# Kernel tuning notes

Hardware: AMD Instinct MI355X
Metric: run time of the kernel (lower is better)

## Reference

```python
import jax, jax.numpy as jnp
import numpy as np

B, TDIM, NDIM, KDIM, VDIM, FDIM, ODIM = 128, 256, 128, 128, 128, 2048, 32


def setup_inputs() -> dict:
    key = jax.random.key(0)
    ks = jax.random.split(key, 14)
    s = 0.02  # small init so sigmoids are not saturated
    return {
        "X":  jax.random.normal(ks[0], (B, TDIM, NDIM), dtype=jnp.float32),
        "Qw": jax.random.normal(ks[1], (NDIM, KDIM), dtype=jnp.float32) * s,
        "Qb": jnp.zeros((KDIM,), dtype=jnp.float32),
        "Kw": jax.random.normal(ks[2], (NDIM, KDIM), dtype=jnp.float32) * s,
        "Kb": jnp.zeros((KDIM,), dtype=jnp.float32),
        "Vw": jax.random.normal(ks[3], (NDIM, VDIM), dtype=jnp.float32) * s,
        "Vb": jnp.zeros((VDIM,), dtype=jnp.float32),
        "W1": jax.random.normal(ks[4], (TDIM * VDIM, FDIM), dtype=jnp.float32) * s,
        "b1": jnp.zeros((FDIM,), dtype=jnp.float32),
        "W2": jax.random.normal(ks[5], (FDIM, FDIM), dtype=jnp.float32) * s,
        "b2": jnp.zeros((FDIM,), dtype=jnp.float32),
        "W3": jax.random.normal(ks[6], (FDIM, ODIM * NDIM), dtype=jnp.float32) * s,
        "b3": jnp.zeros((ODIM * NDIM,), dtype=jnp.float32),
    }


def reference(X, Qw, Qb, Kw, Kb, Vw, Vb, W1, b1, W2, b2, W3, b3):
    # projections [B, T, kdim/vdim]
    q = X @ Qw + Qb
    k = X @ Kw + Kb
    v = X @ Vw + Vb
    # NOTE: original computes softmax(K Q^T) with NO 1/sqrt(d) scaling
    scores = jnp.einsum("btk,bsk->bts", k, q)        # [B, T, T]
    a = jax.nn.softmax(scores, axis=-1)
    r = jnp.einsum("bts,bsv->btv", a, v)              # [B, T, V]
    r = r.reshape(-1, TDIM * VDIM)                    # [B, T*V]
    h = jax.nn.sigmoid(r @ W1 + b1)
    h = jax.nn.sigmoid(h @ W2 + b2)
    return h @ W3 + b3                                # [B, ODIM*NDIM]
```

## Files before the change

kernel.cpp:

```cpp
#include <hip/hip_runtime.h>


#define DI __device__ __forceinline__
#define AS1 __attribute__((address_space(1)))
#define AS3 __attribute__((address_space(3)))

typedef __attribute__((ext_vector_type(4))) float f32x4;
typedef __attribute__((ext_vector_type(8))) short bf16x8;

DI unsigned short f2bf(float f) {
  unsigned int u = __float_as_uint(f);
  u += 0x7fffu + ((u >> 16) & 1u);
  return (unsigned short)(u >> 16);
}

__global__ __launch_bounds__(256) void prep_wt(const float* __restrict__ Qw,
                                               const float* __restrict__ Kw,
                                               const float* __restrict__ Vw,
                                               unsigned short* __restrict__ wT) {
  int gid = blockIdx.x * 256 + threadIdx.x;
  int w  = gid >> 14;
  int j  = gid & 16383;
  int no = j >> 7, ni = j & 127;
  const float* src = (w == 0) ? Qw : (w == 1) ? Kw : Vw;
  wT[gid] = f2bf(src[ni * 128 + no]);
}

__global__ __launch_bounds__(256) void proj_kernel(
    const float* __restrict__ X, const unsigned short* __restrict__ wT,
    const float* __restrict__ Qb, const float* __restrict__ Kb,
    const float* __restrict__ Vb,
    unsigned short* __restrict__ q_ws, unsigned short* __restrict__ k_ws,
    unsigned short* __restrict__ vT_ws) {
  int wv = threadIdx.x >> 6, lane = threadIdx.x & 63;
  int quad = lane >> 4, l15 = lane & 15;
  int R0 = blockIdx.x * 64 + wv * 16;

  bf16x8 af[4];
  const float* xbase = X + (size_t)(R0 + l15) * 128 + quad * 8;
#pragma unroll
  for (int kc = 0; kc < 4; ++kc) {
    f32x4 x0 = *(const f32x4*)(xbase + kc * 32);
    f32x4 x1 = *(const f32x4*)(xbase + kc * 32 + 4);
    bf16x8 a;
#pragma unroll
    for (int j = 0; j < 4; ++j) { a[j] = (short)f2bf(x0[j]); a[4 + j] = (short)f2bf(x1[j]); }
    af[kc] = a;
  }

#pragma unroll
  for (int p = 0; p < 3; ++p) {
    const unsigned short* wt = wT + p * 16384;
    const float* bias = (p == 0) ? Qb : (p == 1) ? Kb : Vb;
#pragma unroll
    for (int nt = 0; nt < 8; ++nt) {
      f32x4 acc = {0.f, 0.f, 0.f, 0.f};
#pragma unroll
      for (int kc = 0; kc < 4; ++kc) {
        bf16x8 b = *(const bf16x8*)(wt + (size_t)(nt * 16 + l15) * 128 + kc * 32 + quad * 8);
        acc = __builtin_amdgcn_mfma_f32_16x16x32_bf16(af[kc], b, acc, 0, 0, 0);
      }
      int no = nt * 16 + l15;
      float bv = bias[no];
#pragma unroll
      for (int r4 = 0; r4 < 4; ++r4) {
        int row = R0 + quad * 4 + r4;
        unsigned short val = f2bf(acc[r4] + bv);
        if (p == 0)      q_ws[(size_t)row * 128 + no] = val;
        else if (p == 1) k_ws[(size_t)row * 128 + no] = val;
        else {
          int bb = row >> 8, t = row & 255;
          vT_ws[((size_t)bb * 128 + no) * 256 + t] = val;
        }
      }
    }
  }
}

__global__ __launch_bounds__(256) void attn_kernel(
    const unsigned short* __restrict__ q_ws, const unsigned short* __restrict__ k_ws,
    const unsigned short* __restrict__ vT_ws, unsigned short* __restrict__ r_ws) {
  __shared__ __align__(16) unsigned short p_lds[4][16 * 264];
  int wv = threadIdx.x >> 6, lane = threadIdx.x & 63;
  int quad = lane >> 4, l15 = lane & 15;
  int b  = blockIdx.x >> 2;
  int t0 = (blockIdx.x & 3) * 64 + wv * 16;

  bf16x8 kf[4];
  const unsigned short* kbase = k_ws + ((size_t)b * 256 + t0 + l15) * 128 + quad * 8;
#pragma unroll
  for (int kc = 0; kc < 4; ++kc) kf[kc] = *(const bf16x8*)(kbase + kc * 32);

  f32x4 sc[16];
#pragma unroll
  for (int st = 0; st < 16; ++st) {
    f32x4 acc = {0.f, 0.f, 0.f, 0.f};
    const unsigned short* qbase = q_ws + ((size_t)b * 256 + st * 16 + l15) * 128 + quad * 8;
#pragma unroll
    for (int kc = 0; kc < 4; ++kc) {
      bf16x8 qf = *(const bf16x8*)(qbase + kc * 32);
      acc = __builtin_amdgcn_mfma_f32_16x16x32_bf16(kf[kc], qf, acc, 0, 0, 0);
    }
    sc[st] = acc;
  }

  float inv[4];
#pragma unroll
  for (int r4 = 0; r4 < 4; ++r4) {
    float m = sc[0][r4];
#pragma unroll
    for (int st = 1; st < 16; ++st) m = fmaxf(m, sc[st][r4]);
#pragma unroll
    for (int d = 1; d < 16; d <<= 1) m = fmaxf(m, __shfl_xor(m, d, 64));
    float s = 0.f;
#pragma unroll
    for (int st = 0; st < 16; ++st) { float e = __expf(sc[st][r4] - m); sc[st][r4] = e; s += e; }
#pragma unroll
    for (int d = 1; d < 16; d <<= 1) s += __shfl_xor(s, d, 64);
    inv[r4] = 1.f / s;
  }

#pragma unroll
  for (int st = 0; st < 16; ++st)
#pragma unroll
    for (int r4 = 0; r4 < 4; ++r4)
      p_lds[wv][(quad * 4 + r4) * 264 + st * 16 + l15] = f2bf(sc[st][r4] * inv[r4]);
  __syncthreads();

  const unsigned short* pbase = &p_lds[wv][l15 * 264 + quad * 8];
#pragma unroll
  for (int vt = 0; vt < 8; ++vt) {
    f32x4 acc = {0.f, 0.f, 0.f, 0.f};
    const unsigned short* vbase = vT_ws + ((size_t)b * 128 + vt * 16 + l15) * 256 + quad * 8;
#pragma unroll
    for (int s8 = 0; s8 < 8; ++s8) {
      bf16x8 pf = *(const bf16x8*)(pbase + s8 * 32);
      bf16x8 vf = *(const bf16x8*)(vbase + s8 * 32);
      acc = __builtin_amdgcn_mfma_f32_16x16x32_bf16(pf, vf, acc, 0, 0, 0);
    }
#pragma unroll
    for (int r4 = 0; r4 < 4; ++r4)
      r_ws[((size_t)b * 256 + t0 + quad * 4 + r4) * 128 + vt * 16 + l15] = f2bf(acc[r4]);
  }
}

__global__ __launch_bounds__(256) void gemm_ksplit(
    const unsigned short* __restrict__ A, int lda,
    const float* __restrict__ B, int ldb,
    float* __restrict__ slab, int ldo, int nChunks) {
  __shared__ __align__(16) unsigned short bt[2][128 * 32];
  const int tid  = threadIdx.x;
  const int wv   = tid >> 6, lane = tid & 63;
  const int quad = lane >> 4, l15 = lane & 15;
  const int n0   = blockIdx.x * 128;
  const long k0  = (long)blockIdx.y * nChunks * 32;
  const int m0   = wv * 32;

  const int kp = tid >> 4;
  const int nq = tid & 15;
  const int gq = kp >> 2;
  const int qd = kp & 3;

  f32x4 acc[2][8];
#pragma unroll
  for (int ms = 0; ms < 2; ++ms)
#pragma unroll
    for (int nt = 0; nt < 8; ++nt) acc[ms][nt] = (f32x4){0.f, 0.f, 0.f, 0.f};

  f32x4 r0, r1, r2, r3;
  auto LOAD = [&](int c) {
    const float* g = B + (size_t)(k0 + c * 32 + 2 * kp) * (size_t)ldb + n0 + nq * 8;
    r0 = *(const f32x4*)(g);
    r1 = *(const f32x4*)(g + 4);
    r2 = *(const f32x4*)(g + ldb);
    r3 = *(const f32x4*)(g + ldb + 4);
  };
  auto WRITE = [&](int pb) {
#pragma unroll
    for (int i = 0; i < 8; ++i) {
      int n = nq * 8 + i;
      float lo = (i < 4) ? r0[i] : r1[i - 4];
      float hi = (i < 4) ? r2[i] : r3[i - 4];
      unsigned int pk = (unsigned int)f2bf(lo) | ((unsigned int)f2bf(hi) << 16);
      int d = ((n >> 1) & 3) ^ ((n >> 3) & 3);
      *(unsigned int*)&bt[pb][n * 32 + ((gq ^ d) << 3) + 2 * qd] = pk;
    }
  };

  const int rb = l15 * 64 + ((quad ^ ((l15 >> 1) & 3) ^ (l15 >> 3)) << 4);

  LOAD(0);
  WRITE(0);
  __syncthreads();

  for (int c = 0; c < nChunks; ++c) {
    const int pb = c & 1;
    if (c + 1 < nChunks) LOAD(c + 1);

    bf16x8 aF[2];
    const unsigned short* abase = A + (size_t)(m0 + l15) * lda + k0 + c * 32 + quad * 8;
    aF[0] = *(const bf16x8*)(abase);
    aF[1] = *(const bf16x8*)(abase + (size_t)16 * lda);

    const char* be = (const char*)&bt[pb][0] + rb;
    const char* bo = (const char*)&bt[pb][0] + (rb ^ 32);
#pragma unroll
    for (int nt = 0; nt < 8; ++nt) {
      bf16x8 bF = *(const bf16x8*)(((nt & 1) ? bo : be) + nt * 1024);
      acc[0][nt] = __builtin_amdgcn_mfma_f32_16x16x32_bf16(aF[0], bF, acc[0][nt], 0, 0, 0);
      acc[1][nt] = __builtin_amdgcn_mfma_f32_16x16x32_bf16(aF[1], bF, acc[1][nt], 0, 0, 0);
    }
    __syncthreads();
    if (c + 1 < nChunks) {
      WRITE(pb ^ 1);
      __syncthreads();
    }
  }

  float* out = slab + (size_t)blockIdx.y * (size_t)ldo * 128;
#pragma unroll
  for (int ms = 0; ms < 2; ++ms)
#pragma unroll
    for (int nt = 0; nt < 8; ++nt)
#pragma unroll
      for (int r4 = 0; r4 < 4; ++r4)
        out[(size_t)(m0 + ms * 16 + quad * 4 + r4) * ldo + n0 + nt * 16 + l15] =
            acc[ms][nt][r4];
}

__global__ __launch_bounds__(256) void reduce_sig(
    const float* __restrict__ slabs, int nslabs, int slabStride,
    const float* __restrict__ bias, int biasMask, unsigned short* __restrict__ outBf) {
  int i = blockIdx.x * 256 + threadIdx.x;
  float s = 0.f;
  for (int y = 0; y < nslabs; ++y) s += slabs[(size_t)y * slabStride + i];
  s += bias[i & biasMask];
  outBf[i] = f2bf(1.f / (1.f + __expf(-s)));
}

__global__ __launch_bounds__(256) void reduce_bias_out(
    const float* __restrict__ slabs, int nslabs, int slabStride,
    const float* __restrict__ bias, int biasMask, float* __restrict__ outF) {
  int i = blockIdx.x * 256 + threadIdx.x;
  float s = 0.f;
  for (int y = 0; y < nslabs; ++y) s += slabs[(size_t)y * slabStride + i];
  outF[i] = s + bias[i & biasMask];
}

extern "C" void kernel_launch(void* const* d_in, const int* in_sizes, int n_in,
                              void* d_out, int out_size, void* d_ws, size_t ws_size,
                              hipStream_t stream) {
  const float* X  = (const float*)d_in[0];
  const float* Qw = (const float*)d_in[1];
  const float* Qb = (const float*)d_in[2];
  const float* Kw = (const float*)d_in[3];
  const float* Kb = (const float*)d_in[4];
  const float* Vw = (const float*)d_in[5];
  const float* Vb = (const float*)d_in[6];
  const float* W1 = (const float*)d_in[7];
  const float* b1 = (const float*)d_in[8];
  const float* W2 = (const float*)d_in[9];
  const float* b2 = (const float*)d_in[10];
  const float* W3 = (const float*)d_in[11];
  const float* b3 = (const float*)d_in[12];

  char* ws = (char*)d_ws;
  unsigned short* wT    = (unsigned short*)(ws + 0);
  unsigned short* r_ws  = (unsigned short*)(ws + 98304);
  unsigned short* q_ws  = (unsigned short*)(ws + 8486912);
  unsigned short* k_ws  = (unsigned short*)(ws + 16875520);
  unsigned short* vT_ws = (unsigned short*)(ws + 25264128);
  float* g1 = (float*)(ws + 8486912);
  unsigned short* h1bf = (unsigned short*)(ws + 42041344);
  float* g2 = (float*)(ws + 8486912);
  unsigned short* h2bf = (unsigned short*)(ws + 42565632);
  float* g3 = (float*)(ws + 8486912);

  prep_wt<<<192, 256, 0, stream>>>(Qw, Kw, Vw, wT);
  proj_kernel<<<512, 256, 0, stream>>>(X, wT, Qb, Kb, Vb, q_ws, k_ws, vT_ws);
  attn_kernel<<<512, 256, 0, stream>>>(q_ws, k_ws, vT_ws, r_ws);
  gemm_ksplit<<<dim3(16, 32), 256, 0, stream>>>(r_ws, 32768, W1, 2048, g1, 2048, 32);
  reduce_sig<<<1024, 256, 0, stream>>>(g1, 32, 262144, b1, 2047, h1bf);
  gemm_ksplit<<<dim3(16, 16), 256, 0, stream>>>(h1bf, 2048, W2, 2048, g2, 2048, 4);
  reduce_sig<<<1024, 256, 0, stream>>>(g2, 16, 262144, b2, 2047, h2bf);
  gemm_ksplit<<<dim3(32, 16), 256, 0, stream>>>(h2bf, 2048, W3, 4096, g3, 4096, 4);
  reduce_bias_out<<<2048, 256, 0, stream>>>(g3, 16, 524288, b3, 4095, (float*)d_out);
}
```

Before: 517.3 us.

## Software-pipeline ksplit GEMM two chunks deep and double W2 k-split

The ksplit GEMM main loop is unrolled by two. It keeps separate register sets for even and odd chunks and prefetches both the A fragments and the B tile two chunks ahead. Plain __syncthreads are replaced by lgkmcnt waits plus raw s_barrier with scheduling fences. The aim is to overlap global loads with MFMA work and to stop the A-fragment loads from stalling the math. The W2 GEMM also moves to 32 k-splits of 2 chunks each for more blocks, at the cost of a larger slab reduction. The loop assumes an even chunk count, and the weaker barriers rely on the manual waitcnt for correctness.

```diff
diff --git a/kernel.cpp b/kernel.cpp
--- a/kernel.cpp
+++ b/kernel.cpp
@@ -2,8 +2,6 @@
 
 
 #define DI __device__ __forceinline__
-#define AS1 __attribute__((address_space(1)))
-#define AS3 __attribute__((address_space(3)))
 
 typedef __attribute__((ext_vector_type(4))) float f32x4;
 typedef __attribute__((ext_vector_type(8))) short bf16x8;
@@ -161,61 +159,85 @@
   const int gq = kp >> 2;
   const int qd = kp & 3;
 
+  const int rb_ = l15 * 64 + ((quad ^ ((l15 >> 1) & 3) ^ (l15 >> 3)) << 4);
+
   f32x4 acc[2][8];
 #pragma unroll
   for (int ms = 0; ms < 2; ++ms)
 #pragma unroll
     for (int nt = 0; nt < 8; ++nt) acc[ms][nt] = (f32x4){0.f, 0.f, 0.f, 0.f};
 
-  f32x4 r0, r1, r2, r3;
-  auto LOAD = [&](int c) {
+  f32x4 e0, e1, e2, e3;
+  f32x4 o0, o1, o2, o3;
+  bf16x8 ae0, ae1;
+  bf16x8 ao0, ao1;
+
+  auto LOADB = [&](int c, f32x4& s0, f32x4& s1, f32x4& s2, f32x4& s3) {
     const float* g = B + (size_t)(k0 + c * 32 + 2 * kp) * (size_t)ldb + n0 + nq * 8;
-    r0 = *(const f32x4*)(g);
-    r1 = *(const f32x4*)(g + 4);
-    r2 = *(const f32x4*)(g + ldb);
-    r3 = *(const f32x4*)(g + ldb + 4);
+    s0 = *(const f32x4*)(g);
+    s1 = *(const f32x4*)(g + 4);
+    s2 = *(const f32x4*)(g + ldb);
+    s3 = *(const f32x4*)(g + ldb + 4);
   };
-  auto WRITE = [&](int pb) {
+  auto LOADA = [&](int c, bf16x8& a0, bf16x8& a1) {
+    const unsigned short* abase = A + (size_t)(m0 + l15) * lda + k0 + c * 32 + quad * 8;
+    a0 = *(const bf16x8*)(abase);
+    a1 = *(const bf16x8*)(abase + (size_t)16 * lda);
+  };
+  auto WRITE = [&](int pb, const f32x4& s0, const f32x4& s1, const f32x4& s2,
+                   const f32x4& s3) {
 #pragma unroll
     for (int i = 0; i < 8; ++i) {
       int n = nq * 8 + i;
-      float lo = (i < 4) ? r0[i] : r1[i - 4];
-      float hi = (i < 4) ? r2[i] : r3[i - 4];
+      float lo = (i < 4) ? s0[i] : s1[i - 4];
+      float hi = (i < 4) ? s2[i] : s3[i - 4];
       unsigned int pk = (unsigned int)f2bf(lo) | ((unsigned int)f2bf(hi) << 16);
       int d = ((n >> 1) & 3) ^ ((n >> 3) & 3);
       *(unsigned int*)&bt[pb][n * 32 + ((gq ^ d) << 3) + 2 * qd] = pk;
     }
   };
-
-  const int rb = l15 * 64 + ((quad ^ ((l15 >> 1) & 3) ^ (l15 >> 3)) << 4);
-
-  LOAD(0);
-  WRITE(0);
-  __syncthreads();
-
-  for (int c = 0; c < nChunks; ++c) {
-    const int pb = c & 1;
-    if (c + 1 < nChunks) LOAD(c + 1);
-
-    bf16x8 aF[2];
-    const unsigned short* abase = A + (size_t)(m0 + l15) * lda + k0 + c * 32 + quad * 8;
-    aF[0] = *(const bf16x8*)(abase);
-    aF[1] = *(const bf16x8*)(abase + (size_t)16 * lda);
-
-    const char* be = (const char*)&bt[pb][0] + rb;
-    const char* bo = (const char*)&bt[pb][0] + (rb ^ 32);
+  auto MFMA8 = [&](int pb, const bf16x8& a0, const bf16x8& a1) {
+    const char* be = (const char*)&bt[pb][0] + rb_;
+    const char* bo = (const char*)&bt[pb][0] + (rb_ ^ 32);
 #pragma unroll
     for (int nt = 0; nt < 8; ++nt) {
       bf16x8 bF = *(const bf16x8*)(((nt & 1) ? bo : be) + nt * 1024);
-      acc[0][nt] = __builtin_amdgcn_mfma_f32_16x16x32_bf16(aF[0], bF, acc[0][nt], 0, 0, 0);
-      acc[1][nt] = __builtin_amdgcn_mfma_f32_16x16x32_bf16(aF[1], bF, acc[1][nt], 0, 0, 0);
-    }
-    __syncthreads();
-    if (c + 1 < nChunks) {
-      WRITE(pb ^ 1);
-      __syncthreads();
-    }
-  }
+      acc[0][nt] = __builtin_amdgcn_mfma_f32_16x16x32_bf16(a0, bF, acc[0][nt], 0, 0, 0);
+      acc[1][nt] = __builtin_amdgcn_mfma_f32_16x16x32_bf16(a1, bF, acc[1][nt], 0, 0, 0);
+    }
+  };
+
+#define BAR_LGKM()                                   \
+  asm volatile("s_waitcnt lgkmcnt(0)" ::: "memory"); \
+  __builtin_amdgcn_sched_barrier(0);                 \
+  __builtin_amdgcn_s_barrier();                      \
+  __builtin_amdgcn_sched_barrier(0)
+
+  LOADB(0, e0, e1, e2, e3);
+  LOADA(0, ae0, ae1);
+  WRITE(0, e0, e1, e2, e3);
+  LOADB(1, o0, o1, o2, o3);
+  LOADA(1, ao0, ao1);
+  BAR_LGKM();
+
+  for (int c = 0; c < nChunks; c += 2) {
+    if (c + 2 < nChunks) LOADB(c + 2, e0, e1, e2, e3);
+    MFMA8(0, ae0, ae1);
+    if (c + 2 < nChunks) LOADA(c + 2, ae0, ae1);
+    BAR_LGKM();
+    WRITE(1, o0, o1, o2, o3);
+    BAR_LGKM();
+
+    if (c + 3 < nChunks) LOADB(c + 3, o0, o1, o2, o3);
+    MFMA8(1, ao0, ao1);
+    if (c + 3 < nChunks) LOADA(c + 3, ao0, ao1);
+    if (c + 2 < nChunks) {
+      BAR_LGKM();
+      WRITE(0, e0, e1, e2, e3);
+      BAR_LGKM();
+    }
+  }
+#undef BAR_LGKM
 
   float* out = slab + (size_t)blockIdx.y * (size_t)ldo * 128;
 #pragma unroll
@@ -281,8 +303,8 @@
   attn_kernel<<<512, 256, 0, stream>>>(q_ws, k_ws, vT_ws, r_ws);
   gemm_ksplit<<<dim3(16, 32), 256, 0, stream>>>(r_ws, 32768, W1, 2048, g1, 2048, 32);
   reduce_sig<<<1024, 256, 0, stream>>>(g1, 32, 262144, b1, 2047, h1bf);
-  gemm_ksplit<<<dim3(16, 16), 256, 0, stream>>>(h1bf, 2048, W2, 2048, g2, 2048, 4);
-  reduce_sig<<<1024, 256, 0, stream>>>(g2, 16, 262144, b2, 2047, h2bf);
+  gemm_ksplit<<<dim3(16, 32), 256, 0, stream>>>(h1bf, 2048, W2, 2048, g2, 2048, 2);
+  reduce_sig<<<1024, 256, 0, stream>>>(g2, 32, 262144, b2, 2047, h2bf);
   gemm_ksplit<<<dim3(32, 16), 256, 0, stream>>>(h2bf, 2048, W3, 4096, g3, 4096, 4);
   reduce_bias_out<<<2048, 256, 0, stream>>>(g3, 16, 524288, b3, 4095, (float*)d_out);
 }
```

New measurement: 524.4 us. About the same (+1.4%).
